# Kernel optimization log

Measured on AMD Instinct MI355X. Metric: run time of the kernel, lower is better.

The kernel has to match this reference:

```python
import jax, jax.numpy as jnp
import numpy as np

EPS = 1e-3
D_MIN, D_MAX = 3.0, 80.0   # z_near, z_far
NUM_FREQS = 6              # -> code dim 3*(1+2*6)=39; 64+39=103 total

N_, NV_, C_, H_, W_ = 4, 4, 64, 96, 320
N_PTS = 50000


def posenc(x):
    # pixelnerf-style positional encoding with include_input, d_in=3
    freqs = jnp.asarray(np.pi * 2.0 ** np.arange(NUM_FREQS), dtype=x.dtype)
    xb = x[..., None, :] * freqs[:, None]                      # [..., F, 3]
    enc = jnp.stack([jnp.sin(xb), jnp.cos(xb)], axis=-2)       # [..., F, 2, 3]
    enc = enc.reshape(x.shape[:-1] + (NUM_FREQS * 2 * 3,))
    return jnp.concatenate([x, enc], axis=-1)                  # [..., 39]


def grid_sample_bilinear_border(fm, xy):
    # fm: [N, C, H, W], xy: [N, P, 2] in [-1, 1]; align_corners=False, border pad
    N, C, H, W = fm.shape
    x = jnp.clip(((xy[..., 0] + 1.0) * W - 1.0) * 0.5, 0.0, W - 1.0)
    y = jnp.clip(((xy[..., 1] + 1.0) * H - 1.0) * 0.5, 0.0, H - 1.0)
    x0 = jnp.floor(x); y0 = jnp.floor(y)
    wx = (x - x0)[:, None, :]; wy = (y - y0)[:, None, :]       # [N, 1, P]
    x0i = x0.astype(jnp.int32); y0i = y0.astype(jnp.int32)
    x1i = jnp.minimum(x0i + 1, W - 1); y1i = jnp.minimum(y0i + 1, H - 1)
    gather = jax.vmap(lambda f, yi, xi: f[:, yi, xi])          # [C, P] per batch
    v00 = gather(fm, y0i, x0i)
    v01 = gather(fm, y0i, x1i)
    v10 = gather(fm, y1i, x0i)
    v11 = gather(fm, y1i, x1i)
    return (v00 * (1 - wx) * (1 - wy) + v01 * wx * (1 - wy)
            + v10 * (1 - wx) * wy + v11 * wx * wy)             # [N, C, P]


def setup_inputs() -> dict:
    key = jax.random.key(0)
    k = jax.random.split(key, 5)
    return {
        "xyz": jax.random.normal(k[0], (N_, N_PTS, 3), jnp.float32),
        "feature_map": jax.random.normal(k[1], (N_, NV_, C_, H_, W_), jnp.float32),
        "poses_w2c": jax.random.normal(k[2], (N_, NV_, 4, 4), jnp.float32),
        "Ks": jax.random.normal(k[3], (N_, NV_, 3, 3), jnp.float32),
        "empty_feature": jax.random.normal(k[4], (C_,), jnp.float32),
    }


def reference(xyz, feature_map, poses_w2c, Ks, empty_feature):
    n, n_pts, _ = xyz.shape
    n, nv, c, h, w = feature_map.shape
    # homogeneous points, project to each camera
    xyzh = jnp.concatenate([xyz, jnp.ones_like(xyz[..., :1])], axis=-1)  # [n,P,4]
    xyz_cam = jnp.einsum('nvij,npj->nvpi', poses_w2c[:, :, :3, :], xyzh)  # [n,nv,P,3]
    proj = jnp.einsum('nvij,nvpj->nvpi', Ks, xyz_cam)                    # [n,nv,P,3]
    z = proj[..., 2:3]
    xy = proj[..., :2] / jnp.maximum(z, EPS)
    invalid = ((z <= EPS) | (xy[..., :1] < -1) | (xy[..., :1] > 1)
               | (xy[..., 1:2] < -1) | (xy[..., 1:2] > 1))               # [n,nv,P,1]
    # code_mode='z', inv_z=True
    z_code = (1.0 / jnp.maximum(z, EPS) - 1.0 / D_MAX) / (1.0 / D_MIN - 1.0 / D_MAX)
    z_code = 2.0 * z_code - 1.0
    code = posenc(jnp.concatenate([xy, z_code], axis=-1))                # [n,nv,P,39]
    code = code.transpose(0, 2, 1, 3)                                    # [n,P,nv,39]
    sampled = grid_sample_bilinear_border(
        feature_map.reshape(n * nv, c, h, w), xy.reshape(n * nv, n_pts, 2))
    sampled = sampled.reshape(n, nv, c, n_pts).transpose(0, 3, 1, 2)     # [n,P,nv,c]
    inv_t = invalid.transpose(0, 2, 1, 3)                                # [n,P,nv,1]
    sampled = jnp.where(inv_t, empty_feature, sampled)                   # learn_empty
    feats = jnp.concatenate([sampled, code], axis=-1)                    # [n,P,nv,103]
    return feats, invalid[..., 0].transpose(0, 2, 1)                     # [n,P,nv]
```

## Files before the change

kernel.cpp:

```cpp
#include <hip/hip_runtime.h>
#include <hip/hip_bf16.h>


#define EPSF 0.001f
constexpr int N_ = 4, NV_ = 4, C_ = 64, H_ = 96, W_ = 320, NPTS = 50000;
constexpr int HW = H_ * W_;
constexpr int FEAT = 103;
constexpr long long FEATS_TOTAL = (long long)N_ * NPTS * NV_ * FEAT;
constexpr size_t TFM_ELEMS = (size_t)N_ * NV_ * HW * C_;
constexpr int PGRP = 64;
constexpr int NBLK = (NPTS + PGRP - 1) / PGRP;
constexpr int TOTAL_GRP = NBLK * N_;
constexpr int PERSIST_BLOCKS = 2048;

template <typename T>
__device__ inline T* rfl_ptr(T* p) {
    unsigned long long u = (unsigned long long)p;
    unsigned lo = __builtin_amdgcn_readfirstlane((unsigned)u);
    unsigned hi = __builtin_amdgcn_readfirstlane((unsigned)(u >> 32));
    return (T*)(((unsigned long long)hi << 32) | lo);
}

__global__ __launch_bounds__(256) void transpose_fm(const float* __restrict__ fm,
                                                    unsigned char* __restrict__ tfm) {
    __shared__ float tile[64][65];
    const int s    = blockIdx.y;
    const int pos0 = blockIdx.x * 64;
    const int t    = threadIdx.x;
    const int lane = t & 63, q = t >> 6;

    const float* src = fm + (size_t)s * C_ * HW;
#pragma unroll
    for (int i = 0; i < 16; ++i) {
        const int c = q * 16 + i;
        tile[c][lane] = src[(size_t)c * HW + pos0 + lane];
    }
    __syncthreads();
    const int g  = t & 15;
    const int pr = t >> 4;
    unsigned int* dstU = (unsigned int*)(tfm + ((size_t)s * HW + pos0) * C_);
#pragma unroll
    for (int i = 0; i < 4; ++i) {
        const int pos = i * 16 + pr;
        const float f0 = tile[4 * g + 0][pos];
        const float f1 = tile[4 * g + 1][pos];
        const float f2 = tile[4 * g + 2][pos];
        const float f3 = tile[4 * g + 3][pos];
        unsigned w = (unsigned)__builtin_amdgcn_cvt_pk_fp8_f32(f0, f1, 0, false);
        w = (unsigned)__builtin_amdgcn_cvt_pk_fp8_f32(f2, f3, (int)w, true);
        dstU[pos * (C_ / 4) + g] = w;
    }
}

template <bool DIRECT>
__global__ __launch_bounds__(256, 8) void mvbts_main(const float* __restrict__ xyz,
                                                     const float* __restrict__ fmapF,
                                                     const unsigned char* __restrict__ fmapB,
                                                     const float* __restrict__ poses,
                                                     const float* __restrict__ Ks,
                                                     const float* __restrict__ ef,
                                                     float* __restrict__ out) {
    __shared__ float  PKall[N_][NV_][21];
    __shared__ int4   offsS[PGRP * NV_];
    __shared__ float4 wS[PGRP * NV_];
    __shared__ float4 auxS[PGRP * NV_];

    const int t    = threadIdx.x;
    const int lane = t & 63;
    const int v    = t >> 6;

    for (int e = t; e < N_ * NV_ * 21; e += 256) {
        const int nn = e / (NV_ * 21), r = e - nn * (NV_ * 21);
        const int vv = r / 21, k = r - vv * 21;
        float val;
        if (k < 12) val = poses[((size_t)(nn * NV_ + vv) * 4 + (k >> 2)) * 4 + (k & 3)];
        else        val = Ks[(size_t)(nn * NV_ + vv) * 9 + (k - 12)];
        PKall[nn][vv][k] = val;
    }

    const int jj = lane - 3;
    const int f6 = (lane >= 3) ? (jj / 6) : 0;
    const int r6 = (lane >= 3) ? (jj - f6 * 6) : 0;
    const int tt = (r6 >= 3) ? 1 : 0;
    const int ci = (lane < 3) ? lane : (r6 - tt * 3);
    const float pf  = (lane < 3) ? 0.f : 3.14159265358979f * (float)(1 << f6);
    const float qtr = (lane >= 3 && tt) ? 1.57079632679490f : 0.f;
    const float efv = ef[lane];

    for (int g = blockIdx.x; g < TOTAL_GRP; g += gridDim.x) {
        const int n  = g / NBLK;
        const int p0 = (g - n * NBLK) * PGRP;
        __syncthreads();

        {
            const int p    = p0 + lane;
            const int p_ld = min(p, NPTS - 1);
            const float X = xyz[((size_t)n * NPTS + p_ld) * 3 + 0];
            const float Y = xyz[((size_t)n * NPTS + p_ld) * 3 + 1];
            const float Z = xyz[((size_t)n * NPTS + p_ld) * 3 + 2];

            const float* pk = PKall[n][v];
            float cam[3], prj[3];
#pragma unroll
            for (int i = 0; i < 3; ++i)
                cam[i] = __fadd_rn(
                           __fadd_rn(__fadd_rn(__fmul_rn(pk[i * 4 + 0], X),
                                               __fmul_rn(pk[i * 4 + 1], Y)),
                                     __fmul_rn(pk[i * 4 + 2], Z)),
                           pk[i * 4 + 3]);
#pragma unroll
            for (int i = 0; i < 3; ++i)
                prj[i] = __fadd_rn(__fadd_rn(__fmul_rn(pk[12 + i * 3 + 0], cam[0]),
                                             __fmul_rn(pk[12 + i * 3 + 1], cam[1])),
                                   __fmul_rn(pk[12 + i * 3 + 2], cam[2]));

            const float pz = prj[2];
            const float zc = fmaxf(pz, EPSF);
            const float x  = __fdiv_rn(prj[0], zc);
            const float y  = __fdiv_rn(prj[1], zc);
            const bool invalid = (pz <= EPSF) || (x < -1.f) || (x > 1.f) || (y < -1.f) || (y > 1.f);

            const float zinv = __fdiv_rn(1.f, zc);
            float z_code = __fdiv_rn(zinv - 0.0125f, (1.f / 3.f - 0.0125f));
            z_code = 2.f * z_code - 1.f;

            float gx = fminf(fmaxf(((x + 1.f) * (float)W_ - 1.f) * 0.5f, 0.f), (float)(W_ - 1));
            float gy = fminf(fmaxf(((y + 1.f) * (float)H_ - 1.f) * 0.5f, 0.f), (float)(H_ - 1));
            const float fx0 = floorf(gx), fy0 = floorf(gy);
            const int x0 = (int)fx0, y0 = (int)fy0;
            const int x1 = min(x0 + 1, W_ - 1), y1 = min(y0 + 1, H_ - 1);
            const float wx = gx - fx0, wy = gy - fy0;
            const float vmask = invalid ? 0.f : 1.f;
            const float owx = 1.f - wx, owy = 1.f - wy;
            const int scl = DIRECT ? 1 : C_;
            int4 o;
            o.x = (y0 * W_ + x0) * scl;
            o.y = (y0 * W_ + x1) * scl;
            o.z = (y1 * W_ + x0) * scl;
            o.w = (y1 * W_ + x1) * scl;
            offsS[t] = o;
            wS[t] = make_float4(vmask * owx * owy, vmask * wx * owy,
                                vmask * owx * wy,  vmask * wx * wy);
            auxS[t] = make_float4(x, y, z_code, invalid ? 1.f : 0.f);

            if (p < NPTS)
                out[FEATS_TOTAL + ((size_t)n * NPTS + p) * NV_ + v] = invalid ? 1.f : 0.f;
        }
        __syncthreads();

        const int s = n * NV_ + v;
        const float* baseF = DIRECT
            ? rfl_ptr(fmapF + ((size_t)s * C_) * HW)
            : nullptr;
        const unsigned char* baseB = DIRECT
            ? nullptr
            : rfl_ptr(fmapB + (size_t)s * HW * C_);
        float* outW = rfl_ptr(out + (((size_t)n * NPTS + p0) * NV_ + v) * FEAT);

        const int nIter = min(PGRP, NPTS - p0);
        unsigned off = 0;
#pragma unroll 2
        for (int i = 0; i < nIter; ++i, off += NV_ * FEAT) {
            const int item = (v << 6) + i;
            const int4   o  = offsS[item];
            const float4 w4 = wS[item];
            const float4 a4 = auxS[item];
            float v00, v01, v10, v11;
            if (DIRECT) {
                const float* bl = baseF + (size_t)lane * HW;
                v00 = bl[o.x]; v01 = bl[o.y]; v10 = bl[o.z]; v11 = bl[o.w];
            } else {
                v00 = __builtin_amdgcn_cvt_f32_fp8((int)baseB[(unsigned)o.x + lane], 0);
                v01 = __builtin_amdgcn_cvt_f32_fp8((int)baseB[(unsigned)o.y + lane], 0);
                v10 = __builtin_amdgcn_cvt_f32_fp8((int)baseB[(unsigned)o.z + lane], 0);
                v11 = __builtin_amdgcn_cvt_f32_fp8((int)baseB[(unsigned)o.w + lane], 0);
            }
            float samp = v00 * w4.x + v01 * w4.y + v10 * w4.z + v11 * w4.w
                       + a4.w * efv;
            outW[off + lane] = samp;

            if (lane < 39) {
                const float b = (ci == 0) ? a4.x : ((ci == 1) ? a4.y : a4.z);
                const float tv = __sinf(b * pf + qtr);
                outW[off + 64 + lane] = (lane < 3) ? b : tv;
            }
        }
    }
}

extern "C" void kernel_launch(void* const* d_in, const int* in_sizes, int n_in,
                              void* d_out, int out_size, void* d_ws, size_t ws_size,
                              hipStream_t stream) {
    const float* xyz   = (const float*)d_in[0];
    const float* fm    = (const float*)d_in[1];
    const float* poses = (const float*)d_in[2];
    const float* Ks    = (const float*)d_in[3];
    const float* ef    = (const float*)d_in[4];
    float* out = (float*)d_out;

    const size_t need = TFM_ELEMS;
    const int nGrid = (TOTAL_GRP < PERSIST_BLOCKS) ? TOTAL_GRP : PERSIST_BLOCKS;
    if (ws_size >= need) {
        unsigned char* tfm = (unsigned char*)d_ws;
        transpose_fm<<<dim3(HW / 64, N_ * NV_), 256, 0, stream>>>(fm, tfm);
        mvbts_main<false><<<dim3(nGrid), 256, 0, stream>>>(xyz, nullptr, tfm, poses, Ks, ef, out);
    } else {
        mvbts_main<true><<<dim3(nGrid), 256, 0, stream>>>(xyz, fm, nullptr, poses, Ks, ef, out);
    }
}
```

Measured before the change: 131.2 us.

## Balance point ranges across blocks and use nontemporal loads and stores

Replaces the group-strided persistent loop with a static split of the flattened batch×points range. Each of the 2048 blocks gets a near-equal contiguous slice, which removes the tail where some blocks processed two 64-point groups and others only one. Batch index and feature-map base are now computed per lane, so a chunk may cross a batch boundary, and the scalar base pointers via readfirstlane are dropped. Output writes and the transpose's feature-map reads become nontemporal to reduce cache pollution from streaming traffic. In exchange, address arithmetic moves into vector registers.

Measured after the change: 165.5 us. 1.26x slower.

```diff
diff --git a/kernel.cpp b/kernel.cpp
--- a/kernel.cpp
+++ b/kernel.cpp
@@ -6,20 +6,10 @@
 constexpr int N_ = 4, NV_ = 4, C_ = 64, H_ = 96, W_ = 320, NPTS = 50000;
 constexpr int HW = H_ * W_;
 constexpr int FEAT = 103;
-constexpr long long FEATS_TOTAL = (long long)N_ * NPTS * NV_ * FEAT;
+constexpr int TOTAL_PTS = N_ * NPTS;
+constexpr long long FEATS_TOTAL = (long long)TOTAL_PTS * NV_ * FEAT;
 constexpr size_t TFM_ELEMS = (size_t)N_ * NV_ * HW * C_;
-constexpr int PGRP = 64;
-constexpr int NBLK = (NPTS + PGRP - 1) / PGRP;
-constexpr int TOTAL_GRP = NBLK * N_;
-constexpr int PERSIST_BLOCKS = 2048;
-
-template <typename T>
-__device__ inline T* rfl_ptr(T* p) {
-    unsigned long long u = (unsigned long long)p;
-    unsigned lo = __builtin_amdgcn_readfirstlane((unsigned)u);
-    unsigned hi = __builtin_amdgcn_readfirstlane((unsigned)(u >> 32));
-    return (T*)(((unsigned long long)hi << 32) | lo);
-}
+constexpr int BLOCKS = 2048;
 
 __global__ __launch_bounds__(256) void transpose_fm(const float* __restrict__ fm,
                                                     unsigned char* __restrict__ tfm) {
@@ -33,7 +23,7 @@
 #pragma unroll
     for (int i = 0; i < 16; ++i) {
         const int c = q * 16 + i;
-        tile[c][lane] = src[(size_t)c * HW + pos0 + lane];
+        tile[c][lane] = __builtin_nontemporal_load(&src[(size_t)c * HW + pos0 + lane]);
     }
     __syncthreads();
     const int g  = t & 15;
@@ -61,9 +51,9 @@
                                                      const float* __restrict__ ef,
                                                      float* __restrict__ out) {
     __shared__ float  PKall[N_][NV_][21];
-    __shared__ int4   offsS[PGRP * NV_];
-    __shared__ float4 wS[PGRP * NV_];
-    __shared__ float4 auxS[PGRP * NV_];
+    __shared__ int4   offsS[256];
+    __shared__ float4 wS[256];
+    __shared__ float4 auxS[256];
 
     const int t    = threadIdx.x;
     const int lane = t & 63;
@@ -87,17 +77,20 @@
     const float qtr = (lane >= 3 && tt) ? 1.57079632679490f : 0.f;
     const float efv = ef[lane];
 
-    for (int g = blockIdx.x; g < TOTAL_GRP; g += gridDim.x) {
-        const int n  = g / NBLK;
-        const int p0 = (g - n * NBLK) * PGRP;
+    const int s0 = (int)(((long long)blockIdx.x * TOTAL_PTS) >> 11);
+    const int s1 = (int)(((long long)(blockIdx.x + 1) * TOTAL_PTS) >> 11);
+
+    for (int c0 = s0; c0 < s1; c0 += 64) {
+        const int cl = min(64, s1 - c0);
         __syncthreads();
 
         {
-            const int p    = p0 + lane;
-            const int p_ld = min(p, NPTS - 1);
-            const float X = xyz[((size_t)n * NPTS + p_ld) * 3 + 0];
-            const float Y = xyz[((size_t)n * NPTS + p_ld) * 3 + 1];
-            const float Z = xyz[((size_t)n * NPTS + p_ld) * 3 + 2];
+            const int P  = c0 + lane;
+            const int Pl = min(P, TOTAL_PTS - 1);
+            const int n  = Pl / NPTS;
+            const float X = xyz[(size_t)Pl * 3 + 0];
+            const float Y = xyz[(size_t)Pl * 3 + 1];
+            const float Z = xyz[(size_t)Pl * 3 + 2];
 
             const float* pk = PKall[n][v];
             float cam[3], prj[3];
@@ -133,56 +126,48 @@
             const float vmask = invalid ? 0.f : 1.f;
             const float owx = 1.f - wx, owy = 1.f - wy;
             const int scl = DIRECT ? 1 : C_;
+            const int sbase = (n * NV_ + v) * (HW * C_);
             int4 o;
-            o.x = (y0 * W_ + x0) * scl;
-            o.y = (y0 * W_ + x1) * scl;
-            o.z = (y1 * W_ + x0) * scl;
-            o.w = (y1 * W_ + x1) * scl;
+            o.x = sbase + (y0 * W_ + x0) * scl;
+            o.y = sbase + (y0 * W_ + x1) * scl;
+            o.z = sbase + (y1 * W_ + x0) * scl;
+            o.w = sbase + (y1 * W_ + x1) * scl;
             offsS[t] = o;
             wS[t] = make_float4(vmask * owx * owy, vmask * wx * owy,
                                 vmask * owx * wy,  vmask * wx * wy);
             auxS[t] = make_float4(x, y, z_code, invalid ? 1.f : 0.f);
 
-            if (p < NPTS)
-                out[FEATS_TOTAL + ((size_t)n * NPTS + p) * NV_ + v] = invalid ? 1.f : 0.f;
+            if (P < s1)
+                __builtin_nontemporal_store(invalid ? 1.f : 0.f,
+                    &out[FEATS_TOTAL + (size_t)P * NV_ + v]);
         }
         __syncthreads();
 
-        const int s = n * NV_ + v;
-        const float* baseF = DIRECT
-            ? rfl_ptr(fmapF + ((size_t)s * C_) * HW)
-            : nullptr;
-        const unsigned char* baseB = DIRECT
-            ? nullptr
-            : rfl_ptr(fmapB + (size_t)s * HW * C_);
-        float* outW = rfl_ptr(out + (((size_t)n * NPTS + p0) * NV_ + v) * FEAT);
-
-        const int nIter = min(PGRP, NPTS - p0);
-        unsigned off = 0;
+        const float* blF = DIRECT ? fmapF + (size_t)lane * HW : nullptr;
+        unsigned off = ((unsigned)c0 * NV_ + v) * FEAT;
 #pragma unroll 2
-        for (int i = 0; i < nIter; ++i, off += NV_ * FEAT) {
+        for (int i = 0; i < cl; ++i, off += NV_ * FEAT) {
             const int item = (v << 6) + i;
             const int4   o  = offsS[item];
             const float4 w4 = wS[item];
             const float4 a4 = auxS[item];
             float v00, v01, v10, v11;
             if (DIRECT) {
-                const float* bl = baseF + (size_t)lane * HW;
-                v00 = bl[o.x]; v01 = bl[o.y]; v10 = bl[o.z]; v11 = bl[o.w];
+                v00 = blF[o.x]; v01 = blF[o.y]; v10 = blF[o.z]; v11 = blF[o.w];
             } else {
-                v00 = __builtin_amdgcn_cvt_f32_fp8((int)baseB[(unsigned)o.x + lane], 0);
-                v01 = __builtin_amdgcn_cvt_f32_fp8((int)baseB[(unsigned)o.y + lane], 0);
-                v10 = __builtin_amdgcn_cvt_f32_fp8((int)baseB[(unsigned)o.z + lane], 0);
-                v11 = __builtin_amdgcn_cvt_f32_fp8((int)baseB[(unsigned)o.w + lane], 0);
+                v00 = __builtin_amdgcn_cvt_f32_fp8((int)fmapB[(unsigned)o.x + lane], 0);
+                v01 = __builtin_amdgcn_cvt_f32_fp8((int)fmapB[(unsigned)o.y + lane], 0);
+                v10 = __builtin_amdgcn_cvt_f32_fp8((int)fmapB[(unsigned)o.z + lane], 0);
+                v11 = __builtin_amdgcn_cvt_f32_fp8((int)fmapB[(unsigned)o.w + lane], 0);
             }
-            float samp = v00 * w4.x + v01 * w4.y + v10 * w4.z + v11 * w4.w
-                       + a4.w * efv;
-            outW[off + lane] = samp;
+            const float samp = v00 * w4.x + v01 * w4.y + v10 * w4.z + v11 * w4.w
+                             + a4.w * efv;
+            __builtin_nontemporal_store(samp, &out[off + lane]);
 
             if (lane < 39) {
                 const float b = (ci == 0) ? a4.x : ((ci == 1) ? a4.y : a4.z);
                 const float tv = __sinf(b * pf + qtr);
-                outW[off + 64 + lane] = (lane < 3) ? b : tv;
+                __builtin_nontemporal_store((lane < 3) ? b : tv, &out[off + 64 + lane]);
             }
         }
     }
@@ -199,12 +184,11 @@
     float* out = (float*)d_out;
 
     const size_t need = TFM_ELEMS;
-    const int nGrid = (TOTAL_GRP < PERSIST_BLOCKS) ? TOTAL_GRP : PERSIST_BLOCKS;
     if (ws_size >= need) {
         unsigned char* tfm = (unsigned char*)d_ws;
         transpose_fm<<<dim3(HW / 64, N_ * NV_), 256, 0, stream>>>(fm, tfm);
-        mvbts_main<false><<<dim3(nGrid), 256, 0, stream>>>(xyz, nullptr, tfm, poses, Ks, ef, out);
+        mvbts_main<false><<<dim3(BLOCKS), 256, 0, stream>>>(xyz, nullptr, tfm, poses, Ks, ef, out);
     } else {
-        mvbts_main<true><<<dim3(nGrid), 256, 0, stream>>>(xyz, fm, nullptr, poses, Ks, ef, out);
+        mvbts_main<true><<<dim3(BLOCKS), 256, 0, stream>>>(xyz, fm, nullptr, poses, Ks, ef, out);
     }
 }
```
